# Performance work log

Hardware: AMD Instinct MI355X
Metric: run time of the kernel (lower is better)

## Reference

```python
import jax, jax.numpy as jnp
import numpy as np
import math

B, C, H, W = 8, 512, 32, 32
NUM_GROUPS = 32
NUM_HEADS = C // 64  # num_head_channels=64 -> 8 heads
EPS = 1e-5


def setup_inputs() -> dict:
    key = jax.random.key(0)
    ks = jax.random.split(key, 7)
    x = jax.random.normal(ks[0], (B, C, H, W), dtype=jnp.float32)
    gn_w = jax.random.uniform(ks[1], (C,), dtype=jnp.float32, minval=0.5, maxval=1.5)
    gn_b = jax.random.normal(ks[2], (C,), dtype=jnp.float32) * 0.1
    qkv_w = jax.random.normal(ks[3], (3 * C, C), dtype=jnp.float32) * 0.02
    qkv_b = jax.random.normal(ks[4], (3 * C,), dtype=jnp.float32) * 0.02
    proj_w = jax.random.normal(ks[5], (C, C), dtype=jnp.float32) * 0.02
    proj_b = jax.random.normal(ks[6], (C,), dtype=jnp.float32) * 0.02
    return {"x": x, "gn_w": gn_w, "gn_b": gn_b, "qkv_w": qkv_w,
            "qkv_b": qkv_b, "proj_w": proj_w, "proj_b": proj_b}


def _group_norm(x, w, b):
    # x: [B, C, L]
    bb, cc, ll = x.shape
    g = x.reshape(bb, NUM_GROUPS, cc // NUM_GROUPS, ll)
    mean = g.mean(axis=(2, 3), keepdims=True)
    var = g.var(axis=(2, 3), keepdims=True)
    g = (g - mean) * jax.lax.rsqrt(var + EPS)
    return g.reshape(bb, cc, ll) * w[None, :, None] + b[None, :, None]


def reference(x, gn_w, gn_b, qkv_w, qkv_b, proj_w, proj_b):
    b, c, h, w = x.shape
    L = h * w
    xf = x.reshape(b, c, L)
    # 1x1 conv1d QKV on normalized input: weight [3C, C]
    qkv = jnp.einsum('oc,bcl->bol', qkv_w, _group_norm(xf, gn_w, gn_b)) + qkv_b[None, :, None]
    ch = c // NUM_HEADS  # per-head channels
    qkv = qkv.reshape(b * NUM_HEADS, 3 * ch, L)
    q, k, v = qkv[:, :ch], qkv[:, ch:2 * ch], qkv[:, 2 * ch:]
    scale = 1.0 / math.sqrt(math.sqrt(ch))
    # [b*H, T, S] scores, softmax over source dim (computed in fp32 per source)
    weight = jnp.einsum('bct,bcs->bts', q * scale, k * scale)
    weight = jax.nn.softmax(weight.astype(jnp.float32), axis=-1).astype(weight.dtype)
    a = jnp.einsum('bts,bcs->bct', weight, v).reshape(b, c, L)
    hproj = jnp.einsum('oc,bcl->bol', proj_w, a) + proj_b[None, :, None]
    return (xf + hproj).reshape(b, c, h, w)
```

## Files before the change

kernel.cpp:

```cpp
#include <hip/hip_runtime.h>
#include <math.h>

#define BB 8
#define CC 512
#define LL 1024
#define GG 32
#define CPG 16
#define NH 8
#define CH 64

typedef unsigned short ushort_t;
typedef __attribute__((ext_vector_type(8))) short short8;
typedef __attribute__((ext_vector_type(4))) float f32x4;

#define SCALE_Q 0.18033688f

__device__ inline ushort_t f2bf(float f) {
  union { float f; unsigned u; } v;
  v.f = f;
  unsigned r = v.u + 0x7FFFu + ((v.u >> 16) & 1u);
  return (ushort_t)(r >> 16);
}

__device__ inline unsigned pack_bf2(float lo, float hi) {
  return __builtin_amdgcn_perm(__float_as_uint(hi), __float_as_uint(lo),
                               0x07060302u);
}

__device__ inline int swz(int r, int k) {
  return r * 64 + ((((k >> 3) ^ (r & 7)) << 3) | (k & 7));
}

__device__ __forceinline__ void g2l16(const void* g, void* l) {
  __builtin_amdgcn_global_load_lds((const unsigned int*)g, (unsigned int*)l,
                                   16, 0, 0);
}

__global__ __launch_bounds__(256) void pre_kernel(
    const float* __restrict__ x, const float* __restrict__ gn_w,
    const float* __restrict__ gn_b, const float* __restrict__ qkv_w,
    const float* __restrict__ proj_w, float* __restrict__ s_bc,
    float* __restrict__ t_bc, ushort_t* __restrict__ wq,
    ushort_t* __restrict__ wp) {
  if (blockIdx.x < BB * GG) {
    int b = blockIdx.x / GG;
    int g = blockIdx.x % GG;
    const float4* xg4 =
        (const float4*)(x + ((size_t)b * CC + (size_t)g * CPG) * LL);
    float sum = 0.f, sq = 0.f;
#pragma unroll
    for (int i = 0; i < 16; ++i) {
      float4 v = xg4[threadIdx.x + i * 256];
      sum += (v.x + v.y) + (v.z + v.w);
      sq += (v.x * v.x + v.y * v.y) + (v.z * v.z + v.w * v.w);
    }
#pragma unroll
    for (int off = 32; off > 0; off >>= 1) {
      sum += __shfl_down(sum, off);
      sq += __shfl_down(sq, off);
    }
    __shared__ float red[8];
    __shared__ float st[2];
    int wave = threadIdx.x >> 6;
    if ((threadIdx.x & 63) == 0) {
      red[wave] = sum;
      red[4 + wave] = sq;
    }
    __syncthreads();
    if (threadIdx.x == 0) {
      float s = red[0] + red[1] + red[2] + red[3];
      float q = red[4] + red[5] + red[6] + red[7];
      float mean = s * (1.f / (CPG * LL));
      float var = q * (1.f / (CPG * LL)) - mean * mean;
      st[0] = mean;
      st[1] = rsqrtf(var + 1e-5f);
    }
    __syncthreads();
    if (threadIdx.x < CPG) {
      int c = g * CPG + threadIdx.x;
      float w = gn_w[c];
      float sc = st[1] * w;
      s_bc[b * CC + c] = sc;
      t_bc[b * CC + c] = gn_b[c] - st[0] * sc;
    }
  } else {
    int cb = blockIdx.x - BB * GG;
    int idx = (cb * 256 + threadIdx.x) * 4;
    const int N1 = 3 * CC * CC;
    float4 v;
    ushort_t* mat;
    int row, k;
    if (idx < N1) {
      v = *(const float4*)(qkv_w + idx);
      row = idx >> 9;
      k = idx & 511;
      mat = wq + (size_t)row * CC;
    } else {
      int j = idx - N1;
      v = *(const float4*)(proj_w + j);
      row = j >> 9;
      k = j & 511;
      mat = wp + (size_t)row * CC;
    }
    int dcol = (k & ~63) | ((((k >> 3) & 7) ^ (row & 7)) << 3) | (k & 7);
    unsigned lo = f2bf(v.x) | ((unsigned)f2bf(v.y) << 16);
    unsigned hi = f2bf(v.z) | ((unsigned)f2bf(v.w) << 16);
    *(uint2*)(mat + dcol) = make_uint2(lo, hi);
  }
}

__global__ __launch_bounds__(256) void xnt_kernel(
    const float* __restrict__ x, const float* __restrict__ s_bc,
    const float* __restrict__ t_bc, ushort_t* __restrict__ xnT) {
  const int b = blockIdx.z;
  const int c0 = blockIdx.y * 64;
  const int l0 = blockIdx.x * 64;
  const int tid = threadIdx.x;
  __shared__ ushort_t Ts[64 * 72];
#pragma unroll
  for (int r4 = 0; r4 < 4; ++r4) {
    int c_local = (tid >> 4) + r4 * 16;
    int l_local = (tid & 15) * 4;
    int c = c0 + c_local;
    float sc = s_bc[b * CC + c], sh = t_bc[b * CC + c];
    float4 v = *(const float4*)(x + ((size_t)b * CC + c) * LL + l0 + l_local);
    float vv[4] = {v.x, v.y, v.z, v.w};
#pragma unroll
    for (int dl = 0; dl < 4; ++dl) {
      int l = l_local + dl;
      int cs = c_local ^ (((l >> 2) & 7) << 3);
      Ts[l * 72 + cs] = f2bf(vv[dl] * sc + sh);
    }
  }
  __syncthreads();
#pragma unroll
  for (int rep = 0; rep < 2; ++rep) {
    int gid = tid + rep * 256;
    int l = gid >> 3, seg = gid & 7;
    uint4 v = *(const uint4*)&Ts[l * 72 + ((seg * 8) ^ (((l >> 2) & 7) << 3))];
    *(uint4*)(xnT + ((size_t)b * LL + l0 + l) * CC + c0 +
              ((seg ^ (l & 7)) << 3)) = v;
  }
}

__global__ __launch_bounds__(384, 3) void qkv_mfma_kernel(
    const ushort_t* __restrict__ wq, const ushort_t* __restrict__ xnT,
    const float* __restrict__ qkv_b, ushort_t* __restrict__ qT,
    ushort_t* __restrict__ kT, ushort_t* __restrict__ vbuf) {
  const int b = blockIdx.z;
  const int m0 = blockIdx.y * 192;
  const int n0 = blockIdx.x * 128;
  const int tid = threadIdx.x;
  const int w = tid >> 6, lane = tid & 63;
  const int col = lane & 15, quad = lane >> 4;
  const int wm = (w >> 1) * 64, wn = (w & 1) * 64;
  __shared__ ushort_t Smem[2 * 20480];
  f32x4 acc[4][4];
  f32x4 z = {0.f, 0.f, 0.f, 0.f};
#pragma unroll
  for (int i = 0; i < 4; ++i)
#pragma unroll
    for (int j = 0; j < 4; ++j) acc[i][j] = z;

  const ushort_t* arow = wq + (size_t)m0 * CC;
  const ushort_t* brow = xnT + ((size_t)b * LL + n0) * CC;

  auto stage = [&](int bb, int k0) {
    ushort_t* As = Smem + bb * 20480;
    ushort_t* Bs = As + 12288;
#pragma unroll
    for (int j = 0; j < 4; ++j) {
      int e = (j * 6 + w) * 512 + lane * 8;
      g2l16(arow + (size_t)(e >> 6) * CC + k0 + (e & 63),
            As + (j * 6 + w) * 512);
    }
    if (w < 4) {
#pragma unroll
      for (int j = 0; j < 4; ++j) {
        int e = (j * 4 + w) * 512 + lane * 8;
        g2l16(brow + (size_t)(e >> 6) * CC + k0 + (e & 63),
              Bs + (j * 4 + w) * 512);
      }
    }
  };

  stage(0, 0);
  __syncthreads();
  int cur = 0;
  for (int step = 0; step < 8; ++step) {
    if (step < 7) stage(cur ^ 1, (step + 1) * 64);
    const ushort_t* As = Smem + cur * 20480;
    const ushort_t* Bs = As + 12288;
#pragma unroll
    for (int kk = 0; kk < 2; ++kk) {
      short8 af[4], bf[4];
#pragma unroll
      for (int mi = 0; mi < 4; ++mi)
        af[mi] = *(const short8*)&As[swz(wm + mi * 16 + col, kk * 32 + quad * 8)];
#pragma unroll
      for (int ni = 0; ni < 4; ++ni)
        bf[ni] = *(const short8*)&Bs[swz(wn + ni * 16 + col, kk * 32 + quad * 8)];
#pragma unroll
      for (int mi = 0; mi < 4; ++mi)
#pragma unroll
        for (int ni = 0; ni < 4; ++ni)
          acc[mi][ni] = __builtin_amdgcn_mfma_f32_16x16x32_bf16(
              af[mi], bf[ni], acc[mi][ni], 0, 0, 0);
    }
    __syncthreads();
    cur ^= 1;
  }
  const int ci_w = w >> 1;
  ushort_t* Tile = Smem + ci_w * 8192;
  if (ci_w < 2) {
    const float sc = (ci_w == 0) ? SCALE_Q : 1.f;
#pragma unroll
    for (int mi = 0; mi < 4; ++mi) {
      int mg = m0 + wm + mi * 16 + quad * 4;
      float b0 = qkv_b[mg + 0], b1 = qkv_b[mg + 1];
      float b2 = qkv_b[mg + 2], b3 = qkv_b[mg + 3];
      int ch = mi * 16 + quad * 4;
#pragma unroll
      for (int ni = 0; ni < 4; ++ni) {
        int lloc = wn + ni * 16 + col;
        float v0 = (acc[mi][ni][0] + b0) * sc;
        float v1 = (acc[mi][ni][1] + b1) * sc;
        float v2 = (acc[mi][ni][2] + b2) * sc;
        float v3 = (acc[mi][ni][3] + b3) * sc;
        int chs = ch ^ ((lloc & 7) << 3);
        *(uint2*)&Tile[lloc * 64 + chs] =
            make_uint2(pack_bf2(v0, v1), pack_bf2(v2, v3));
      }
    }
  } else {
#pragma unroll
    for (int mi = 0; mi < 4; ++mi)
#pragma unroll
      for (int r = 0; r < 4; ++r) {
        int ch = mi * 16 + quad * 4 + r;
        float bias = qkv_b[m0 + wm + ch];
#pragma unroll
        for (int ni = 0; ni < 4; ++ni) {
          int lloc = wn + ni * 16 + col;
          Tile[ch * 128 + lloc] =
              (ushort_t)(__float_as_uint(acc[mi][ni][r] + bias) >> 16);
        }
      }
  }
  __syncthreads();
  const int head = blockIdx.y;
  const int bh = b * NH + head;
#pragma unroll
  for (int ci = 0; ci < 3; ++ci) {
    ushort_t* T2 = Smem + ci * 8192;
    if (ci < 2) {
      ushort_t* dst = (ci == 0) ? qT : kT;
#pragma unroll
      for (int it = 0; it < 3; ++it) {
        int idx = tid + it * 384;
        if (idx < 1024) {
          int l = idx >> 3, seg = idx & 7;
          uint4 v = *(const uint4*)&T2[l * 64 + seg * 8];
          *(uint4*)(dst + ((size_t)bh * LL + n0 + l) * CH + seg * 8) = v;
        }
      }
    } else {
#pragma unroll
      for (int it = 0; it < 3; ++it) {
        int idx = tid + it * 384;
        if (idx < 1024) {
          int ch = idx >> 4, lseg = idx & 15;
          uint4 v = *(const uint4*)&T2[ch * 128 + lseg * 8];
          int g = lseg & 7, blk = lseg >> 3;
          *(uint4*)(vbuf + ((size_t)bh * CH + ch) * LL + n0 + blk * 64 +
                    ((g ^ (ch & 7)) << 3)) = v;
        }
      }
    }
  }
}

__global__ __launch_bounds__(256) void attn_mfma_kernel(
    const ushort_t* __restrict__ qT, const ushort_t* __restrict__ kT,
    const ushort_t* __restrict__ vbuf, ushort_t* __restrict__ abuf) {
  const int Bx = blockIdx.x;
  const int bh = (Bx & 7) * 8 + ((Bx >> 3) >> 4);
  const int t0g = ((Bx >> 3) & 15) * 64;
  const int b = bh >> 3, h = bh & 7;
  const int tid = threadIdx.x;
  const int w = tid >> 6, lane = tid & 63;
  const int col = lane & 15, quad = lane >> 4;
  const int strip = w * 16;
  __shared__ ushort_t Ps[64 * 64];
  __shared__ ushort_t Ksm[2][64 * 64];
  __shared__ ushort_t Vsm[2][64 * 64];

  const ushort_t* kbase = kT + (size_t)bh * LL * CH;
  const ushort_t* vbase = vbuf + (size_t)bh * CH * LL;
  const int eb = w * 1024 + lane * 8;

#pragma unroll
  for (int i = 0; i < 2; ++i) {
    int ee = eb + i * 512;
    g2l16(kbase + ee, &Ksm[0][w * 1024 + i * 512]);
    g2l16(vbase + (size_t)(ee >> 6) * LL + (ee & 63),
          &Vsm[0][w * 1024 + i * 512]);
  }
  const ushort_t* qtile = qT + ((size_t)bh * LL + t0g) * CH;
  short8 bq[2];
  bq[0] = *(const short8*)&qtile[swz(strip + col, quad * 8)];
  bq[1] = *(const short8*)&qtile[swz(strip + col, 32 + quad * 8)];

  float m_s = 0.f, lsum = 0.f;
  f32x4 oacc[4];
  f32x4 z = {0.f, 0.f, 0.f, 0.f};
#pragma unroll
  for (int ci = 0; ci < 4; ++ci) oacc[ci] = z;
  __syncthreads();

  int cur = 0;
  for (int it = 0; it < 16; ++it) {
    if (it < 15) {
      const ushort_t* kn = kbase + (size_t)(it + 1) * 64 * CH;
      const ushort_t* vn = vbase + (it + 1) * 64;
#pragma unroll
      for (int i = 0; i < 2; ++i) {
        int ee = eb + i * 512;
        g2l16(kn + ee, &Ksm[cur ^ 1][w * 1024 + i * 512]);
        g2l16(vn + (size_t)(ee >> 6) * LL + (ee & 63),
              &Vsm[cur ^ 1][w * 1024 + i * 512]);
      }
    }
    const ushort_t* Kc = Ksm[cur];
    const ushort_t* Vc = Vsm[cur];
    f32x4 sacc[4];
#pragma unroll
    for (int si = 0; si < 4; ++si) sacc[si] = z;
    __builtin_amdgcn_s_setprio(1);
#pragma unroll
    for (int kk = 0; kk < 2; ++kk)
#pragma unroll
      for (int si = 0; si < 4; ++si) {
        short8 ak = *(const short8*)&Kc[swz(si * 16 + col, kk * 32 + quad * 8)];
        sacc[si] = __builtin_amdgcn_mfma_f32_16x16x32_bf16(ak, bq[kk],
                                                           sacc[si], 0, 0, 0);
      }
    __builtin_amdgcn_s_setprio(0);
    if (it == 0) {
      float mx = sacc[0][0];
#pragma unroll
      for (int si = 0; si < 4; ++si)
#pragma unroll
        for (int r = 0; r < 4; ++r) mx = fmaxf(mx, sacc[si][r]);
      mx = fmaxf(mx, __shfl_xor(mx, 16));
      mx = fmaxf(mx, __shfl_xor(mx, 32));
      m_s = mx;
    }
#pragma unroll
    for (int si = 0; si < 4; ++si) {
      float p0 = __builtin_amdgcn_exp2f(sacc[si][0] - m_s);
      float p1 = __builtin_amdgcn_exp2f(sacc[si][1] - m_s);
      float p2 = __builtin_amdgcn_exp2f(sacc[si][2] - m_s);
      float p3 = __builtin_amdgcn_exp2f(sacc[si][3] - m_s);
      lsum += (p0 + p1) + (p2 + p3);
      int base = swz(strip + col, si * 16 + quad * 4);
      *(unsigned*)&Ps[base] = pack_bf2(p0, p1);
      *(unsigned*)&Ps[base + 2] = pack_bf2(p2, p3);
    }
    __builtin_amdgcn_s_setprio(1);
#pragma unroll
    for (int kk = 0; kk < 2; ++kk) {
      short8 ap = *(const short8*)&Ps[swz(strip + col, kk * 32 + quad * 8)];
#pragma unroll
      for (int ci = 0; ci < 4; ++ci) {
        short8 bv = *(const short8*)&Vc[swz(ci * 16 + col, kk * 32 + quad * 8)];
        oacc[ci] = __builtin_amdgcn_mfma_f32_16x16x32_bf16(ap, bv, oacc[ci],
                                                           0, 0, 0);
      }
    }
    __builtin_amdgcn_s_setprio(0);
    __syncthreads();
    cur ^= 1;
  }
  lsum += __shfl_xor(lsum, 16);
  lsum += __shfl_xor(lsum, 32);
  float linv[4];
#pragma unroll
  for (int r = 0; r < 4; ++r)
    linv[r] = 1.f / __shfl(lsum, (lane & 48) | (quad * 4 + r), 64);
#pragma unroll
  for (int r = 0; r < 4; ++r) {
    int l = t0g + strip + quad * 4 + r;
#pragma unroll
    for (int ci = 0; ci < 4; ++ci) {
      int cl = ci * 16 + col;
      int dcol = ((((cl >> 3) ^ (l & 7)) << 3) | (cl & 7));
      abuf[((size_t)b * LL + l) * CC + h * CH + dcol] =
          f2bf(oacc[ci][r] * linv[r]);
    }
  }
}

__global__ __launch_bounds__(256) void proj_mfma_kernel(
    const ushort_t* __restrict__ wp, const ushort_t* __restrict__ abuf,
    const float* __restrict__ proj_b, const float* __restrict__ x,
    float* __restrict__ out) {
  const int b = blockIdx.z;
  const int m0 = blockIdx.y * 64;
  const int n0 = blockIdx.x * 128;
  const int tid = threadIdx.x;
  const int w = tid >> 6, lane = tid & 63;
  const int col = lane & 15, quad = lane >> 4;
  const int wm = (w >> 1) * 32, wn = (w & 1) * 64;
  __shared__ ushort_t Smem[2 * 12288];
  f32x4 acc[2][4];
  f32x4 z = {0.f, 0.f, 0.f, 0.f};
#pragma unroll
  for (int i = 0; i < 2; ++i)
#pragma unroll
    for (int j = 0; j < 4; ++j) acc[i][j] = z;

  const ushort_t* arow = wp + (size_t)m0 * CC;
  const ushort_t* brow = abuf + ((size_t)b * LL + n0) * CC;

  auto stage = [&](int bb, int k0) {
    ushort_t* As = Smem + bb * 12288;
    ushort_t* Bs = As + 4096;
#pragma unroll
    for (int j = 0; j < 2; ++j) {
      int e = (j * 4 + w) * 512 + lane * 8;
      g2l16(arow + (size_t)(e >> 6) * CC + k0 + (e & 63),
            As + (j * 4 + w) * 512);
    }
#pragma unroll
    for (int j = 0; j < 4; ++j) {
      int e = (j * 4 + w) * 512 + lane * 8;
      g2l16(brow + (size_t)(e >> 6) * CC + k0 + (e & 63),
            Bs + (j * 4 + w) * 512);
    }
  };

  stage(0, 0);
  __syncthreads();
  int cur = 0;
  for (int step = 0; step < 8; ++step) {
    if (step < 7) stage(cur ^ 1, (step + 1) * 64);
    const ushort_t* As = Smem + cur * 12288;
    const ushort_t* Bs = As + 4096;
#pragma unroll
    for (int kk = 0; kk < 2; ++kk) {
      short8 af[2], bf[4];
#pragma unroll
      for (int mi = 0; mi < 2; ++mi)
        af[mi] = *(const short8*)&As[swz(wm + mi * 16 + col, kk * 32 + quad * 8)];
#pragma unroll
      for (int ni = 0; ni < 4; ++ni)
        bf[ni] = *(const short8*)&Bs[swz(wn + ni * 16 + col, kk * 32 + quad * 8)];
#pragma unroll
      for (int mi = 0; mi < 2; ++mi)
#pragma unroll
        for (int ni = 0; ni < 4; ++ni)
          acc[mi][ni] = __builtin_amdgcn_mfma_f32_16x16x32_bf16(
              af[mi], bf[ni], acc[mi][ni], 0, 0, 0);
    }
    __syncthreads();
    cur ^= 1;
  }
#pragma unroll
  for (int mi = 0; mi < 2; ++mi)
#pragma unroll
    for (int r = 0; r < 4; ++r) {
      int o = m0 + wm + mi * 16 + quad * 4 + r;
      float bias = proj_b[o];
#pragma unroll
      for (int ni = 0; ni < 4; ++ni) {
        int l = n0 + wn + ni * 16 + col;
        size_t off = ((size_t)b * CC + o) * LL + l;
        out[off] = x[off] + bias + acc[mi][ni][r];
      }
    }
}

extern "C" void kernel_launch(void* const* d_in, const int* in_sizes, int n_in,
                              void* d_out, int out_size, void* d_ws,
                              size_t ws_size, hipStream_t stream) {
  const float* x = (const float*)d_in[0];
  const float* gn_w = (const float*)d_in[1];
  const float* gn_b = (const float*)d_in[2];
  const float* qkv_w = (const float*)d_in[3];
  const float* qkv_b = (const float*)d_in[4];
  const float* proj_w = (const float*)d_in[5];
  const float* proj_b = (const float*)d_in[6];
  float* out = (float*)d_out;

  char* ws = (char*)d_ws;
  float* s_bc = (float*)ws;
  float* t_bc = s_bc + BB * CC;
  ushort_t* wq = (ushort_t*)(t_bc + BB * CC);
  ushort_t* wp = wq + (size_t)3 * CC * CC;
  ushort_t* xnT = wp + (size_t)CC * CC;
  ushort_t* qT = xnT + (size_t)BB * LL * CC;
  ushort_t* kT = qT + (size_t)BB * NH * LL * CH;
  ushort_t* vb = kT + (size_t)BB * NH * LL * CH;
  ushort_t* abuf = vb + (size_t)BB * NH * LL * CH;

  pre_kernel<<<BB * GG + 1024, 256, 0, stream>>>(x, gn_w, gn_b, qkv_w, proj_w,
                                                 s_bc, t_bc, wq, wp);
  xnt_kernel<<<dim3(LL / 64, CC / 64, BB), 256, 0, stream>>>(x, s_bc, t_bc,
                                                             xnT);
  qkv_mfma_kernel<<<dim3(LL / 128, 1536 / 192, BB), 384, 0, stream>>>(
      wq, xnT, qkv_b, qT, kT, vb);
  attn_mfma_kernel<<<dim3(1024), 256, 0, stream>>>(qT, kT, vb, abuf);
  proj_mfma_kernel<<<dim3(LL / 128, CC / 64, BB), 256, 0, stream>>>(
      wp, abuf, proj_b, x, out);
}
```

Baseline: 143.9 us.

## Use 32x32x16 MFMA in attention with register-resident P via permlane32 swap

```diff
diff --git a/kernel.cpp b/kernel.cpp
--- a/kernel.cpp
+++ b/kernel.cpp
@@ -12,6 +12,7 @@
 typedef unsigned short ushort_t;
 typedef __attribute__((ext_vector_type(8))) short short8;
 typedef __attribute__((ext_vector_type(4))) float f32x4;
+typedef __attribute__((ext_vector_type(16))) float f32x16;
 
 #define SCALE_Q 0.18033688f
 
@@ -284,14 +285,12 @@
     const ushort_t* __restrict__ qT, const ushort_t* __restrict__ kT,
     const ushort_t* __restrict__ vbuf, ushort_t* __restrict__ abuf) {
   const int Bx = blockIdx.x;
-  const int bh = (Bx & 7) * 8 + ((Bx >> 3) >> 4);
-  const int t0g = ((Bx >> 3) & 15) * 64;
+  const int bh = (Bx & 7) * 8 + ((Bx >> 3) >> 3);
+  const int t0g = ((Bx >> 3) & 7) * 128;
   const int b = bh >> 3, h = bh & 7;
   const int tid = threadIdx.x;
   const int w = tid >> 6, lane = tid & 63;
-  const int col = lane & 15, quad = lane >> 4;
-  const int strip = w * 16;
-  __shared__ ushort_t Ps[64 * 64];
+  const int ln31 = lane & 31, hi = lane >> 5;
   __shared__ ushort_t Ksm[2][64 * 64];
   __shared__ ushort_t Vsm[2][64 * 64];
 
@@ -307,15 +306,17 @@
           &Vsm[0][w * 1024 + i * 512]);
   }
   const ushort_t* qtile = qT + ((size_t)bh * LL + t0g) * CH;
-  short8 bq[2];
-  bq[0] = *(const short8*)&qtile[swz(strip + col, quad * 8)];
-  bq[1] = *(const short8*)&qtile[swz(strip + col, 32 + quad * 8)];
+  short8 bq[4];
+#pragma unroll
+  for (int j = 0; j < 4; ++j)
+    bq[j] = *(const short8*)&qtile[swz(w * 32 + ln31, j * 16 + hi * 8)];
 
   float m_s = 0.f, lsum = 0.f;
-  f32x4 oacc[4];
-  f32x4 z = {0.f, 0.f, 0.f, 0.f};
-#pragma unroll
-  for (int ci = 0; ci < 4; ++ci) oacc[ci] = z;
+  f32x16 oacc[2];
+  f32x16 zz = {0.f, 0.f, 0.f, 0.f, 0.f, 0.f, 0.f, 0.f,
+               0.f, 0.f, 0.f, 0.f, 0.f, 0.f, 0.f, 0.f};
+  oacc[0] = zz;
+  oacc[1] = zz;
   __syncthreads();
 
   int cur = 0;
@@ -333,70 +334,80 @@
     }
     const ushort_t* Kc = Ksm[cur];
     const ushort_t* Vc = Vsm[cur];
-    f32x4 sacc[4];
-#pragma unroll
-    for (int si = 0; si < 4; ++si) sacc[si] = z;
+    f32x16 sacc[2];
+    sacc[0] = zz;
+    sacc[1] = zz;
     __builtin_amdgcn_s_setprio(1);
 #pragma unroll
-    for (int kk = 0; kk < 2; ++kk)
-#pragma unroll
-      for (int si = 0; si < 4; ++si) {
-        short8 ak = *(const short8*)&Kc[swz(si * 16 + col, kk * 32 + quad * 8)];
-        sacc[si] = __builtin_amdgcn_mfma_f32_16x16x32_bf16(ak, bq[kk],
-                                                           sacc[si], 0, 0, 0);
+    for (int sq = 0; sq < 2; ++sq)
+#pragma unroll
+      for (int j = 0; j < 4; ++j) {
+        short8 ak = *(const short8*)&Kc[swz(sq * 32 + ln31, j * 16 + hi * 8)];
+        sacc[sq] = __builtin_amdgcn_mfma_f32_32x32x16_bf16(ak, bq[j],
+                                                           sacc[sq], 0, 0, 0);
       }
     __builtin_amdgcn_s_setprio(0);
     if (it == 0) {
       float mx = sacc[0][0];
 #pragma unroll
-      for (int si = 0; si < 4; ++si)
-#pragma unroll
-        for (int r = 0; r < 4; ++r) mx = fmaxf(mx, sacc[si][r]);
-      mx = fmaxf(mx, __shfl_xor(mx, 16));
-      mx = fmaxf(mx, __shfl_xor(mx, 32));
+      for (int sq = 0; sq < 2; ++sq)
+#pragma unroll
+        for (int r = 0; r < 16; ++r) mx = fmaxf(mx, sacc[sq][r]);
+#pragma unroll
+      for (int off = 32; off > 0; off >>= 1) mx = fmaxf(mx, __shfl_xor(mx, off));
       m_s = mx;
     }
-#pragma unroll
-    for (int si = 0; si < 4; ++si) {
-      float p0 = __builtin_amdgcn_exp2f(sacc[si][0] - m_s);
-      float p1 = __builtin_amdgcn_exp2f(sacc[si][1] - m_s);
-      float p2 = __builtin_amdgcn_exp2f(sacc[si][2] - m_s);
-      float p3 = __builtin_amdgcn_exp2f(sacc[si][3] - m_s);
-      lsum += (p0 + p1) + (p2 + p3);
-      int base = swz(strip + col, si * 16 + quad * 4);
-      *(unsigned*)&Ps[base] = pack_bf2(p0, p1);
-      *(unsigned*)&Ps[base + 2] = pack_bf2(p2, p3);
+    short8 pf[4];
+#pragma unroll
+    for (int sq = 0; sq < 2; ++sq) {
+      float p[16];
+#pragma unroll
+      for (int r = 0; r < 16; ++r) {
+        p[r] = __builtin_amdgcn_exp2f(sacc[sq][r] - m_s);
+        lsum += p[r];
+      }
+      unsigned d0[4], d1[4];
+#pragma unroll
+      for (int q = 0; q < 4; ++q) {
+        d0[q] = pack_bf2(p[q * 4 + 0], p[q * 4 + 1]);
+        d1[q] = pack_bf2(p[q * 4 + 2], p[q * 4 + 3]);
+      }
+#pragma unroll
+      for (int m = 0; m < 2; ++m) {
+        unsigned x0 = d0[m * 2], y0 = d0[m * 2 + 1];
+        unsigned x1 = d1[m * 2], y1 = d1[m * 2 + 1];
+        asm volatile("v_permlane32_swap_b32 %0, %1" : "+v"(x0), "+v"(y0));
+        asm volatile("v_permlane32_swap_b32 %0, %1" : "+v"(x1), "+v"(y1));
+        union { uint4 u; short8 s; } fu;
+        fu.u = make_uint4(x0, x1, y0, y1);
+        pf[sq * 2 + m] = fu.s;
+      }
     }
     __builtin_amdgcn_s_setprio(1);
 #pragma unroll
-    for (int kk = 0; kk < 2; ++kk) {
-      short8 ap = *(const short8*)&Ps[swz(strip + col, kk * 32 + quad * 8)];
-#pragma unroll
-      for (int ci = 0; ci < 4; ++ci) {
-        short8 bv = *(const short8*)&Vc[swz(ci * 16 + col, kk * 32 + quad * 8)];
-        oacc[ci] = __builtin_amdgcn_mfma_f32_16x16x32_bf16(ap, bv, oacc[ci],
-                                                           0, 0, 0);
-      }
-    }
+    for (int cq = 0; cq < 2; ++cq)
+#pragma unroll
+      for (int ks = 0; ks < 4; ++ks) {
+        short8 bv = *(const short8*)&Vc[swz(cq * 32 + ln31, ks * 16 + hi * 8)];
+        oacc[cq] = __builtin_amdgcn_mfma_f32_32x32x16_bf16(pf[ks], bv,
+                                                           oacc[cq], 0, 0, 0);
+      }
     __builtin_amdgcn_s_setprio(0);
     __syncthreads();
     cur ^= 1;
   }
-  lsum += __shfl_xor(lsum, 16);
   lsum += __shfl_xor(lsum, 32);
-  float linv[4];
-#pragma unroll
-  for (int r = 0; r < 4; ++r)
-    linv[r] = 1.f / __shfl(lsum, (lane & 48) | (quad * 4 + r), 64);
-#pragma unroll
-  for (int r = 0; r < 4; ++r) {
-    int l = t0g + strip + quad * 4 + r;
-#pragma unroll
-    for (int ci = 0; ci < 4; ++ci) {
-      int cl = ci * 16 + col;
-      int dcol = ((((cl >> 3) ^ (l & 7)) << 3) | (cl & 7));
-      abuf[((size_t)b * LL + l) * CC + h * CH + dcol] =
-          f2bf(oacc[ci][r] * linv[r]);
+#pragma unroll
+  for (int r = 0; r < 16; ++r) {
+    int tl = (r & 3) + 8 * (r >> 2) + 4 * hi;
+    float li = 1.f / __shfl(lsum, tl, 64);
+    int lg = t0g + w * 32 + tl;
+#pragma unroll
+    for (int cq = 0; cq < 2; ++cq) {
+      int cl = cq * 32 + ln31;
+      int dcol = ((((cl >> 3) ^ (lg & 7)) << 3) | (cl & 7));
+      abuf[((size_t)b * LL + lg) * CC + h * CH + dcol] =
+          f2bf(oacc[cq][r] * li);
     }
   }
 }
@@ -510,7 +521,7 @@
                                                              xnT);
   qkv_mfma_kernel<<<dim3(LL / 128, 1536 / 192, BB), 384, 0, stream>>>(
       wq, xnT, qkv_b, qT, kT, vb);
-  attn_mfma_kernel<<<dim3(1024), 256, 0, stream>>>(qT, kT, vb, abuf);
+  attn_mfma_kernel<<<dim3(512), 256, 0, stream>>>(qT, kT, vb, abuf);
   proj_mfma_kernel<<<dim3(LL / 128, CC / 64, BB), 256, 0, stream>>>(
       wp, abuf, proj_b, x, out);
 }
```

Result: faster. 139.5 us (-3.0%).
